# Optimization experiments

Measured on AMD Instinct MI355X. Metric: run time of the kernel, lower is better.

Reference implementation:

```python
import jax, jax.numpy as jnp
import numpy as np

G = 16          # horizontal stripes
K = 4           # latents per stripe
TEMP = 0.125
TOPK_RATIO = 0.125
GATE_THR = 0.05
EPS = 1e-6
KSZ = 3


def setup_inputs() -> dict:
    key = jax.random.key(0)
    k1, k2 = jax.random.split(key)
    x = jax.random.normal(k1, (64, 256, 64, 44), dtype=jnp.float32)
    latent_basis = jax.random.normal(k2, (G, K, 256), dtype=jnp.float32)
    return {"x": x, "latent_basis": latent_basis}


def _avg_pool3(x):
    # x: [n, g, c, sh, w]; 3x3 avg pool, stride 1, pad 1, count_include_pad=True
    s = jax.lax.reduce_window(x, 0.0, jax.lax.add,
                              (1, 1, 1, KSZ, KSZ), (1, 1, 1, 1, 1),
                              [(0, 0), (0, 0), (0, 0), (1, 1), (1, 1)])
    return s / float(KSZ * KSZ)


def _l2norm(v, axis=-1):
    return v / jnp.maximum(jnp.linalg.norm(v, axis=axis, keepdims=True), 1e-12)


def reference(x, latent_basis):
    n, c, h, w = x.shape
    sh = h // G
    p = sh * w
    # split into horizontal stripes: [n, g, c, sh, w]
    xr = x.reshape(n, c, G, sh, w).transpose(0, 2, 1, 3, 4)
    support_feat = _avg_pool3(xr)
    feat_flat = xr.transpose(0, 1, 3, 4, 2).reshape(n, G, p, c)          # ngpc
    support_flat = support_feat.transpose(0, 1, 3, 4, 2).reshape(n, G, p, c)

    # active mask from detached feature energy
    e = jax.lax.stop_gradient(xr).astype(jnp.float32)
    fe = jnp.mean(e * e, axis=2)                                          # n g sh w
    fe = fe / jnp.maximum(jnp.max(fe, axis=(-2, -1), keepdims=True), EPS)
    active = (fe > GATE_THR).astype(jnp.float32)
    fallback = (fe > 0).astype(jnp.float32)
    use_fb = jnp.sum(active, axis=(-2, -1), keepdims=True) <= 0
    active = jnp.where(use_fb, fallback, active).reshape(n, G, p)

    # cosine-similarity routing
    sfn = _l2norm(support_flat)
    lbn = _l2norm(latent_basis)                                           # g k c
    logits = jnp.einsum('ngpc,gkc->ngpk', sfn, lbn) / TEMP
    route_prob = jax.nn.softmax(logits, axis=-1)
    support = route_prob * active[..., None]                              # n g p k
    pool_w = support / jnp.maximum(jnp.sum(support, axis=2, keepdims=True), EPS)
    tokens = jnp.einsum('ngpk,ngpc->ngkc', pool_w, feat_flat)
    tokens = tokens.transpose(0, 3, 1, 2).reshape(n, c, G * K)            # n c (g k)

    # top-k presence
    kk = max(1, min(p, int(p * TOPK_RATIO)))
    topv, _ = jax.lax.top_k(support.transpose(0, 1, 3, 2), kk)            # n g k kk
    presence = jnp.mean(topv, axis=-1).reshape(n, G * K)
    presence = presence / jnp.maximum(jnp.sum(presence, axis=1, keepdims=True), EPS)

    # scatter per-stripe maps back into full-resolution zero tensors
    eye = jnp.eye(G, dtype=support.dtype)
    loc_s = support.reshape(n, G, sh, w, K).transpose(0, 1, 4, 2, 3)      # n g k sh w
    loc_p = pool_w.reshape(n, G, sh, w, K).transpose(0, 1, 4, 2, 3)
    smap = jnp.einsum('ngksw,gG->ngkGsw', loc_s, eye).reshape(n, G * K, h, w)
    pmap = jnp.einsum('ngksw,gG->ngkGsw', loc_p, eye).reshape(n, G * K, h, w)
    support_flat_global = smap.transpose(0, 2, 3, 1).reshape(n, h * w, G * K)
    pool_weights_flat_global = pmap.transpose(0, 2, 3, 1).reshape(n, h * w, G * K)

    return (tokens.astype(x.dtype), presence.astype(x.dtype),
            support_flat_global.astype(x.dtype), pool_weights_flat_global.astype(x.dtype))
```

## Files before the change

kernel.cpp:

```cpp
#include <hip/hip_runtime.h>
#include <math.h>

#define GG   16
#define KK   4
#define NN   64
#define CC   256
#define SHH  4
#define WW   44
#define PP   176
#define HWSZ 2816
#define CHW  720896
#define TOPKK 22

template<int CTRL, int RMASK>
__device__ __forceinline__ float dpp0(float v) {
    return __int_as_float(__builtin_amdgcn_update_dpp(
        0, __float_as_int(v), CTRL, RMASK, 0xF, true));
}
__device__ __forceinline__ float nbrL(float v) { return dpp0<0x138, 0xF>(v); }
__device__ __forceinline__ float nbrR(float v) { return dpp0<0x130, 0xF>(v); }

__device__ __forceinline__ float wave_sum63(float v) {
    v += dpp0<0x111, 0xF>(v);
    v += dpp0<0x112, 0xF>(v);
    v += dpp0<0x114, 0xF>(v);
    v += dpp0<0x118, 0xF>(v);
    v += dpp0<0x142, 0xA>(v);
    v += dpp0<0x143, 0xC>(v);
    return v;
}
__device__ __forceinline__ float bcast63(float v) {
    return __int_as_float(__builtin_amdgcn_readlane(__float_as_int(v), 63));
}
__device__ __forceinline__ float wave_sum_all(float v) { return bcast63(wave_sum63(v)); }

__device__ __forceinline__ float wave_max_nn(float v) {
    v = fmaxf(v, dpp0<0x111, 0xF>(v));
    v = fmaxf(v, dpp0<0x112, 0xF>(v));
    v = fmaxf(v, dpp0<0x114, 0xF>(v));
    v = fmaxf(v, dpp0<0x118, 0xF>(v));
    v = fmaxf(v, dpp0<0x142, 0xA>(v));
    v = fmaxf(v, dpp0<0x143, 0xC>(v));
    return bcast63(v);
}

__global__ __launch_bounds__(512, 8) void routing_kernel(
    const float* __restrict__ x, const float* __restrict__ lb_raw,
    float* __restrict__ sup_ws, float* __restrict__ pw_ws,
    float* __restrict__ pres_ws) {
    const int g = blockIdx.x;
    const int n = blockIdx.y;
    const int tid = threadIdx.x;
    const int w = __builtin_amdgcn_readfirstlane(tid >> 6);
    const int lane = tid & 63;
    const bool al = lane < WW;

    __shared__ float4 pd[8][PP];
    __shared__ float2 pnf[8][PP];
    __shared__ float4 lbn_lds[CC];
    __shared__ float redA[4], redB[4], zred[4][4];
    float4* sup4 = pd[2];
    float4* pw4  = pd[4];

    if (w < 4) {
        const float* row = lb_raw + ((size_t)g * KK + w) * CC;
        float v0 = row[lane], v1 = row[lane + 64], v2 = row[lane + 128], v3 = row[lane + 192];
        float ss = v0 * v0 + v1 * v1 + v2 * v2 + v3 * v3;
        float tot = wave_sum_all(ss);
        float sc = (1.0f / 9.0f) / fmaxf(sqrtf(tot), 1e-12f);
        float* dst = (float*)lbn_lds;
        dst[lane * 4 + w]         = v0 * sc;
        dst[(lane + 64) * 4 + w]  = v1 * sc;
        dst[(lane + 128) * 4 + w] = v2 * sc;
        dst[(lane + 192) * 4 + w] = v3 * sc;
    }
    __syncthreads();

    const float* xb = x + (size_t)n * CHW + g * PP;
    const int c0 = w * 32;

    float4 dk[4];
    float nr[4] = {0, 0, 0, 0}, fe[4] = {0, 0, 0, 0};
    #pragma unroll
    for (int s = 0; s < 4; ++s) dk[s] = make_float4(0, 0, 0, 0);

    const float* xp = xb + (size_t)c0 * HWSZ + lane;
    float c0r = 0, c1r = 0, c2r = 0, c3r = 0;
    float n0r = 0, n1r = 0, n2r = 0, n3r = 0;
    if (al) {
        c0r = xp[0]; c1r = xp[44]; c2r = xp[88]; c3r = xp[132];
        n0r = xp[HWSZ]; n1r = xp[HWSZ + 44]; n2r = xp[HWSZ + 88]; n3r = xp[HWSZ + 132];
    }
    xp += 2 * HWSZ;
    #pragma unroll 1
    for (int i = 0; i < 32; ++i) {
        float f0 = 0, f1 = 0, f2 = 0, f3 = 0;
        if (i < 30 && al) { f0 = xp[0]; f1 = xp[44]; f2 = xp[88]; f3 = xp[132]; }
        xp += HWSZ;
        float4 lbv = lbn_lds[c0 + i];
        fe[0] += c0r * c0r; fe[1] += c1r * c1r; fe[2] += c2r * c2r; fe[3] += c3r * c3r;
        float h0 = c0r + nbrL(c0r) + nbrR(c0r);
        float h1 = c1r + nbrL(c1r) + nbrR(c1r);
        float h2 = c2r + nbrL(c2r) + nbrR(c2r);
        float h3 = c3r + nbrL(c3r) + nbrR(c3r);
        float p0 = h0 + h1;
        float p1 = p0 + h2;
        float t23 = h2 + h3;
        float p2 = h1 + t23;
        float p3 = t23;
        nr[0] += p0 * p0; nr[1] += p1 * p1; nr[2] += p2 * p2; nr[3] += p3 * p3;
        dk[0].x += p0 * lbv.x; dk[0].y += p0 * lbv.y; dk[0].z += p0 * lbv.z; dk[0].w += p0 * lbv.w;
        dk[1].x += p1 * lbv.x; dk[1].y += p1 * lbv.y; dk[1].z += p1 * lbv.z; dk[1].w += p1 * lbv.w;
        dk[2].x += p2 * lbv.x; dk[2].y += p2 * lbv.y; dk[2].z += p2 * lbv.z; dk[2].w += p2 * lbv.w;
        dk[3].x += p3 * lbv.x; dk[3].y += p3 * lbv.y; dk[3].z += p3 * lbv.z; dk[3].w += p3 * lbv.w;
        c0r = n0r; c1r = n1r; c2r = n2r; c3r = n3r;
        n0r = f0; n1r = f1; n2r = f2; n3r = f3;
    }
    if (al) {
        #pragma unroll
        for (int s = 0; s < 4; ++s) {
            pd[w][s * 44 + lane]  = dk[s];
            pnf[w][s * 44 + lane] = make_float2(nr[s], fe[s]);
        }
    }
    __syncthreads();

    if (tid < PP) {
        float4 a = pd[0][tid];
        #pragma unroll
        for (int ww = 1; ww < 8; ++ww) {
            float4 b = pd[ww][tid];
            a.x += b.x; a.y += b.y; a.z += b.z; a.w += b.w;
        }
        pd[0][tid] = a;
    } else if (tid >= 256 && tid < 256 + PP) {
        const int p = tid - 256;
        float2 a = pnf[0][p];
        #pragma unroll
        for (int ww = 1; ww < 8; ++ww) {
            float2 b = pnf[ww][p];
            a.x += b.x; a.y += b.y;
        }
        pnf[0][p] = a;
    }
    __syncthreads();

    const int s4 = w & 3;
    const int pix = s4 * 44 + (al ? lane : 0);
    float4 dv = pd[0][pix];
    float2 nf = pnf[0][pix];
    float nrm = nf.x;
    float fev = nf.y * (1.0f / 256.0f);

    float fmw = wave_max_nn(al ? fev : 0.0f);
    if (w < 4 && lane == 0) redA[s4] = fmw;
    __syncthreads();
    float femax = fmaxf(fmaxf(redA[0], redA[1]), fmaxf(redA[2], redA[3]));
    float den = fmaxf(femax, 1e-6f);
    bool pa = al && ((fev / den) > 0.05f);
    unsigned long long bl = __ballot((int)pa);
    if (w < 4 && lane == 0) redB[s4] = (float)__popcll(bl);
    __syncthreads();
    float cnt = redB[0] + redB[1] + redB[2] + redB[3];
    float actv = pa ? 1.0f : 0.0f;
    if (cnt <= 0.0f) actv = (al && (fev > 0.0f)) ? 1.0f : 0.0f;

    float inv = 72.0f / fmaxf(sqrtf(nrm), 9e-12f);
    float L0 = dv.x * inv, L1 = dv.y * inv, L2 = dv.z * inv, L3 = dv.w * inv;
    float mx = fmaxf(fmaxf(L0, L1), fmaxf(L2, L3));
    float e0 = expf(L0 - mx), e1 = expf(L1 - mx), e2 = expf(L2 - mx), e3 = expf(L3 - mx);
    float esum = e0 + e1 + e2 + e3;
    float sc = actv / esum;
    float s0 = e0 * sc, s1 = e1 * sc, s2 = e2 * sc, s3 = e3 * sc;

    float z0 = wave_sum63(s0), z1 = wave_sum63(s1), z2 = wave_sum63(s2), z3 = wave_sum63(s3);
    if (w < 4 && lane == 63) { zred[s4][0] = z0; zred[s4][1] = z1; zred[s4][2] = z2; zred[s4][3] = z3; }
    __syncthreads();
    float Z0 = zred[0][0] + zred[1][0] + zred[2][0] + zred[3][0];
    float Z1 = zred[0][1] + zred[1][1] + zred[2][1] + zred[3][1];
    float Z2 = zred[0][2] + zred[1][2] + zred[2][2] + zred[3][2];
    float Z3 = zred[0][3] + zred[1][3] + zred[2][3] + zred[3][3];
    float q0 = s0 / fmaxf(Z0, 1e-6f);
    float q1 = s1 / fmaxf(Z1, 1e-6f);
    float q2 = s2 / fmaxf(Z2, 1e-6f);
    float q3 = s3 / fmaxf(Z3, 1e-6f);

    if (w < 4 && al) {
        float4 sv = make_float4(s0, s1, s2, s3);
        float4 qv = make_float4(q0, q1, q2, q3);
        sup4[pix] = sv;
        pw4[pix]  = qv;
        const size_t wsb = (size_t)(n * GG + g) * PP + pix;
        ((float4*)sup_ws)[wsb] = sv;
        ((float4*)pw_ws)[wsb]  = qv;
    }
    __syncthreads();

    if (w < 4) {
        const float* supf = (const float*)sup4;
        const int k = w;
        float v0 = supf[lane * 4 + k];
        float v1 = supf[(lane + 64) * 4 + k];
        float v2 = (lane < PP - 128) ? supf[(lane + 128) * 4 + k] : -1e30f;
        float tks = 0.0f;
        for (int it = 0; it < TOPKK; ++it) {
            float lm = fmaxf(v0, fmaxf(v1, v2));
            float M = wave_max_nn(lm);
            tks += M;
            unsigned long long mk = __ballot((int)(lm == M));
            int src = __ffsll(mk) - 1;
            if (lane == src) {
                if (v0 == M)      v0 = -1e30f;
                else if (v1 == M) v1 = -1e30f;
                else              v2 = -1e30f;
            }
        }
        if (lane == 0) pres_ws[(size_t)n * 64 + g * KK + k] = tks * (1.0f / (float)TOPKK);
    }
}

__global__ __launch_bounds__(512, 8) void tokscat_kernel(
    const float* __restrict__ x,
    const float4* __restrict__ sup_ws4, const float4* __restrict__ pw_ws4,
    float* __restrict__ tok_out, float4* __restrict__ outS, float4* __restrict__ outP) {
    const int g = blockIdx.x;
    const int n = blockIdx.y;
    const int tid = threadIdx.x;
    const int w = __builtin_amdgcn_readfirstlane(tid >> 6);
    const int lane = tid & 63;

    __shared__ float4 ls[PP], lp[PP];
    const size_t wsb = (size_t)(n * GG + g) * PP;
    if (tid < PP) ls[tid] = sup_ws4[wsb + tid];
    else if (tid >= 256 && tid < 256 + PP) lp[tid - 256] = pw_ws4[wsb + tid - 256];
    __syncthreads();

    {
        const size_t obase = ((size_t)n * HWSZ + (size_t)g * PP) * 16;
        const float4 z = make_float4(0, 0, 0, 0);
        #pragma unroll 1
        for (int j = tid; j < PP * 16; j += 512) {
            const int px = j >> 4, q = j & 15;
            const bool hit = (q == g);
            outS[obase + j] = hit ? ls[px] : z;
            outP[obase + j] = hit ? lp[px] : z;
        }
    }

    {
        float4 pwa = lp[lane];
        float4 pwb = lp[lane + 64];
        float4 pwc = (lane < 48) ? lp[lane + 128] : make_float4(0, 0, 0, 0);
        const int cb = w * 32;
        const float* xp = x + (size_t)n * CHW + g * PP + (size_t)cb * HWSZ + lane;
        float* tokg = tok_out + (size_t)n * CC * 64 + g * KK + (size_t)cb * 64;

        float a0 = xp[0];
        float a1 = xp[64];
        float a2 = (lane < 48) ? xp[128] : 0.0f;
        xp += HWSZ;
        #pragma unroll 1
        for (int i = 0; i < 32; ++i) {
            float b0 = 0, b1 = 0, b2 = 0;
            if (i < 31) {
                b0 = xp[0]; b1 = xp[64];
                if (lane < 48) b2 = xp[128];
            }
            xp += HWSZ;
            float t0 = a0 * pwa.x + a1 * pwb.x + a2 * pwc.x;
            float t1 = a0 * pwa.y + a1 * pwb.y + a2 * pwc.y;
            float t2 = a0 * pwa.z + a1 * pwb.z + a2 * pwc.z;
            float t3 = a0 * pwa.w + a1 * pwb.w + a2 * pwc.w;
            t0 = wave_sum63(t0); t1 = wave_sum63(t1); t2 = wave_sum63(t2); t3 = wave_sum63(t3);
            if (lane == 63) {
                *(float4*)(tokg + (size_t)i * 64) = make_float4(t0, t1, t2, t3);
            }
            a0 = b0; a1 = b1; a2 = b2;
        }
    }
}

__global__ __launch_bounds__(64) void presence_kernel(
    const float* __restrict__ pres_ws, float* __restrict__ outp) {
    const int n = blockIdx.x;
    const int lane = threadIdx.x;
    float v = pres_ws[(size_t)n * 64 + lane];
    float tot = wave_sum_all(v);
    outp[(size_t)n * 64 + lane] = v / fmaxf(tot, 1e-6f);
}

extern "C" void kernel_launch(void* const* d_in, const int* in_sizes, int n_in,
                              void* d_out, int out_size, void* d_ws, size_t ws_size,
                              hipStream_t stream) {
    const float* x = (const float*)d_in[0];
    const float* lb = (const float*)d_in[1];
    float* ws = (float*)d_ws;
    float* pres_ws = ws;
    float* sup_ws  = pres_ws + 4096;
    float* pw_ws   = sup_ws + 720896;

    float* out = (float*)d_out;
    float* tok  = out;
    float* pres = out + 1048576;
    float* outS = out + 1052672;
    float* outP = outS + 11534336;

    routing_kernel<<<dim3(GG, NN), 512, 0, stream>>>(x, lb, sup_ws, pw_ws, pres_ws);
    tokscat_kernel<<<dim3(GG, NN), 512, 0, stream>>>(
        x, (const float4*)sup_ws, (const float4*)pw_ws, tok, (float4*)outS, (float4*)outP);
    presence_kernel<<<NN, 64, 0, stream>>>(pres_ws, pres);
}
```

Baseline: 351.7 us.

## Fuse scatter output writes into routing kernel and split token reduction finer

Result: faster. 342.3 us (-2.7%).

```diff
diff --git a/kernel.cpp b/kernel.cpp
--- a/kernel.cpp
+++ b/kernel.cpp
@@ -46,8 +46,8 @@
 
 __global__ __launch_bounds__(512, 8) void routing_kernel(
     const float* __restrict__ x, const float* __restrict__ lb_raw,
-    float* __restrict__ sup_ws, float* __restrict__ pw_ws,
-    float* __restrict__ pres_ws) {
+    float* __restrict__ pw_ws, float* __restrict__ pres_ws,
+    float4* __restrict__ outS, float4* __restrict__ outP) {
     const int g = blockIdx.x;
     const int n = blockIdx.y;
     const int tid = threadIdx.x;
@@ -190,9 +190,7 @@
         float4 qv = make_float4(q0, q1, q2, q3);
         sup4[pix] = sv;
         pw4[pix]  = qv;
-        const size_t wsb = (size_t)(n * GG + g) * PP + pix;
-        ((float4*)sup_ws)[wsb] = sv;
-        ((float4*)pw_ws)[wsb]  = qv;
+        ((float4*)pw_ws)[(size_t)(n * GG + g) * PP + pix] = qv;
     }
     __syncthreads();
 
@@ -217,23 +215,6 @@
         }
         if (lane == 0) pres_ws[(size_t)n * 64 + g * KK + k] = tks * (1.0f / (float)TOPKK);
     }
-}
-
-__global__ __launch_bounds__(512, 8) void tokscat_kernel(
-    const float* __restrict__ x,
-    const float4* __restrict__ sup_ws4, const float4* __restrict__ pw_ws4,
-    float* __restrict__ tok_out, float4* __restrict__ outS, float4* __restrict__ outP) {
-    const int g = blockIdx.x;
-    const int n = blockIdx.y;
-    const int tid = threadIdx.x;
-    const int w = __builtin_amdgcn_readfirstlane(tid >> 6);
-    const int lane = tid & 63;
-
-    __shared__ float4 ls[PP], lp[PP];
-    const size_t wsb = (size_t)(n * GG + g) * PP;
-    if (tid < PP) ls[tid] = sup_ws4[wsb + tid];
-    else if (tid >= 256 && tid < 256 + PP) lp[tid - 256] = pw_ws4[wsb + tid - 256];
-    __syncthreads();
 
     {
         const size_t obase = ((size_t)n * HWSZ + (size_t)g * PP) * 16;
@@ -242,41 +223,51 @@
         for (int j = tid; j < PP * 16; j += 512) {
             const int px = j >> 4, q = j & 15;
             const bool hit = (q == g);
-            outS[obase + j] = hit ? ls[px] : z;
-            outP[obase + j] = hit ? lp[px] : z;
-        }
-    }
-
-    {
-        float4 pwa = lp[lane];
-        float4 pwb = lp[lane + 64];
-        float4 pwc = (lane < 48) ? lp[lane + 128] : make_float4(0, 0, 0, 0);
-        const int cb = w * 32;
-        const float* xp = x + (size_t)n * CHW + g * PP + (size_t)cb * HWSZ + lane;
-        float* tokg = tok_out + (size_t)n * CC * 64 + g * KK + (size_t)cb * 64;
-
-        float a0 = xp[0];
-        float a1 = xp[64];
-        float a2 = (lane < 48) ? xp[128] : 0.0f;
+            outS[obase + j] = hit ? sup4[px] : z;
+            outP[obase + j] = hit ? pw4[px]  : z;
+        }
+    }
+}
+
+__global__ __launch_bounds__(256, 8) void token_kernel(
+    const float* __restrict__ x, const float* __restrict__ pw_ws,
+    float* __restrict__ tok_out) {
+    const int g = blockIdx.x & 15;
+    const int chunk = blockIdx.x >> 4;
+    const int n = blockIdx.y;
+    const int w = __builtin_amdgcn_readfirstlane(threadIdx.x >> 6);
+    const int lane = threadIdx.x & 63;
+
+    const float4* pwq = (const float4*)pw_ws + (size_t)(n * GG + g) * PP;
+    float4 pwa = pwq[lane];
+    float4 pwb = pwq[lane + 64];
+    float4 pwc = (lane < 48) ? pwq[lane + 128] : make_float4(0, 0, 0, 0);
+
+    const int cb = chunk * 64 + w * 16;
+    const float* xp = x + (size_t)n * CHW + g * PP + (size_t)cb * HWSZ + lane;
+    float* tokg = tok_out + (size_t)n * CC * 64 + g * KK + (size_t)cb * 64;
+
+    float a0 = xp[0];
+    float a1 = xp[64];
+    float a2 = (lane < 48) ? xp[128] : 0.0f;
+    xp += HWSZ;
+    #pragma unroll 1
+    for (int i = 0; i < 16; ++i) {
+        float b0 = 0, b1 = 0, b2 = 0;
+        if (i < 15) {
+            b0 = xp[0]; b1 = xp[64];
+            if (lane < 48) b2 = xp[128];
+        }
         xp += HWSZ;
-        #pragma unroll 1
-        for (int i = 0; i < 32; ++i) {
-            float b0 = 0, b1 = 0, b2 = 0;
-            if (i < 31) {
-                b0 = xp[0]; b1 = xp[64];
-                if (lane < 48) b2 = xp[128];
-            }
-            xp += HWSZ;
-            float t0 = a0 * pwa.x + a1 * pwb.x + a2 * pwc.x;
-            float t1 = a0 * pwa.y + a1 * pwb.y + a2 * pwc.y;
-            float t2 = a0 * pwa.z + a1 * pwb.z + a2 * pwc.z;
-            float t3 = a0 * pwa.w + a1 * pwb.w + a2 * pwc.w;
-            t0 = wave_sum63(t0); t1 = wave_sum63(t1); t2 = wave_sum63(t2); t3 = wave_sum63(t3);
-            if (lane == 63) {
-                *(float4*)(tokg + (size_t)i * 64) = make_float4(t0, t1, t2, t3);
-            }
-            a0 = b0; a1 = b1; a2 = b2;
-        }
+        float t0 = a0 * pwa.x + a1 * pwb.x + a2 * pwc.x;
+        float t1 = a0 * pwa.y + a1 * pwb.y + a2 * pwc.y;
+        float t2 = a0 * pwa.z + a1 * pwb.z + a2 * pwc.z;
+        float t3 = a0 * pwa.w + a1 * pwb.w + a2 * pwc.w;
+        t0 = wave_sum63(t0); t1 = wave_sum63(t1); t2 = wave_sum63(t2); t3 = wave_sum63(t3);
+        if (lane == 63) {
+            *(float4*)(tokg + (size_t)i * 64) = make_float4(t0, t1, t2, t3);
+        }
+        a0 = b0; a1 = b1; a2 = b2;
     }
 }
 
@@ -296,8 +287,7 @@
     const float* lb = (const float*)d_in[1];
     float* ws = (float*)d_ws;
     float* pres_ws = ws;
-    float* sup_ws  = pres_ws + 4096;
-    float* pw_ws   = sup_ws + 720896;
+    float* pw_ws   = pres_ws + 4096;
 
     float* out = (float*)d_out;
     float* tok  = out;
@@ -305,8 +295,8 @@
     float* outS = out + 1052672;
     float* outP = outS + 11534336;
 
-    routing_kernel<<<dim3(GG, NN), 512, 0, stream>>>(x, lb, sup_ws, pw_ws, pres_ws);
-    tokscat_kernel<<<dim3(GG, NN), 512, 0, stream>>>(
-        x, (const float4*)sup_ws, (const float4*)pw_ws, tok, (float4*)outS, (float4*)outP);
+    routing_kernel<<<dim3(GG, NN), 512, 0, stream>>>(
+        x, lb, pw_ws, pres_ws, (float4*)outS, (float4*)outP);
+    token_kernel<<<dim3(GG * 4, NN), 256, 0, stream>>>(x, pw_ws, tok);
     presence_kernel<<<NN, 64, 0, stream>>>(pres_ws, pres);
 }
```
